# Optimization experiments

Measured on AMD Instinct MI355X. Metric: run time of the kernel, lower is better.

The kernel has to match this reference:

```python
import jax, jax.numpy as jnp
import numpy as np

HIDDEN = 150

def setup_inputs() -> dict:
    key = jax.random.key(0)
    ks = jax.random.split(key, 6)
    B, N, E = 1, 512, 256
    G = 3 * E  # gij_dim = 768
    embeds = jax.random.normal(ks[0], (B, N, E), dtype=jnp.float32)
    mention_scores = jax.random.normal(ks[1], (B, N, 1), dtype=jnp.float32)
    W1 = jax.random.normal(ks[2], (G, HIDDEN), dtype=jnp.float32) * (1.0 / np.sqrt(G))
    b1 = jnp.zeros((HIDDEN,), dtype=jnp.float32)
    W2 = jax.random.normal(ks[3], (HIDDEN, HIDDEN), dtype=jnp.float32) * (1.0 / np.sqrt(HIDDEN))
    b2 = jnp.zeros((HIDDEN,), dtype=jnp.float32)
    W3 = jax.random.normal(ks[4], (HIDDEN, 1), dtype=jnp.float32) * (1.0 / np.sqrt(HIDDEN))
    b3 = jnp.zeros((1,), dtype=jnp.float32)
    return {"batch_document_span_embeds": embeds, "mention_scores": mention_scores,
            "W1": W1, "b1": b1, "W2": W2, "b2": b2, "W3": W3, "b3": b3}


def reference(batch_document_span_embeds, mention_scores, W1, b1, W2, b2, W3, b3):
    g = batch_document_span_embeds            # [B, N, E]
    gi = g[:, :, None, :]                     # span_1 broadcast -> [B, N, 1, E]
    gj = g[:, None, :, :]                     # span_2 broadcast -> [B, 1, N, E]
    B, N, E = g.shape
    # pairwise feature cat((s1, s2, s1*s2)) -> [B, N, N, 3E]
    pair = jnp.concatenate([
        jnp.broadcast_to(gi, (B, N, N, E)),
        jnp.broadcast_to(gj, (B, N, N, E)),
        gi * gj,
    ], axis=-1)
    # small MLP score (dropout is inference-mode identity)
    h = jax.nn.relu(pair @ W1 + b1)           # [B, N, N, 150]
    h = jax.nn.relu(h @ W2 + b2)              # [B, N, N, 150]
    s = h @ W3 + b3                           # [B, N, N, 1]
    # mean of (mention_i, mention_j, pair_ij)
    out = (mention_scores[:, :, None, :] + mention_scores[:, None, :, :] + s) / 3.0
    return out                                # [B, N, N, 1]
```

## Files before the change

kernel.cpp:

```cpp
#include <hip/hip_runtime.h>

#define N  512
#define E  256
#define H  150
#define HP 160
#define JB 64
#define NCH (N / JB)

typedef __attribute__((ext_vector_type(8))) short short8;
typedef __attribute__((ext_vector_type(4))) float f32x4;
typedef __attribute__((ext_vector_type(4))) unsigned uint4v;
typedef __attribute__((ext_vector_type(2))) unsigned uint2v;

__device__ __forceinline__ unsigned short f2bf(float f) {
    unsigned u = __float_as_uint(f);
    u += 0x7fffu + ((u >> 16) & 1u);
    return (unsigned short)(u >> 16);
}
__device__ __forceinline__ unsigned pkbf(float a, float b) {
    return (unsigned)f2bf(a) | ((unsigned)f2bf(b) << 16);
}

__global__ __launch_bounds__(192) void precompute_ab(
    const float* __restrict__ g, const float* __restrict__ W1,
    const float* __restrict__ b1, float* __restrict__ wsA,
    unsigned short* __restrict__ wsB)
{
    const int i0  = blockIdx.x * 4;
    const int tid = threadIdx.x;
    __shared__ float gi[4][E];
    for (int idx = tid; idx < 4 * E; idx += 192) gi[idx >> 8][idx & 255] = g[i0 * E + idx];
    __syncthreads();
    const int h = tid;
    if (h < HP) {
        float a[4] = {0, 0, 0, 0}, b[4] = {0, 0, 0, 0};
        if (h < H) {
            for (int e = 0; e < E; ++e) {
                const float wa = W1[e * H + h];
                const float wb = W1[(E + e) * H + h];
#pragma unroll
                for (int qq = 0; qq < 4; ++qq) {
                    a[qq] = fmaf(gi[qq][e], wa, a[qq]);
                    b[qq] = fmaf(gi[qq][e], wb, b[qq]);
                }
            }
            const float bb = b1[h];
#pragma unroll
            for (int qq = 0; qq < 4; ++qq) a[qq] += bb;
        }
#pragma unroll
        for (int qq = 0; qq < 4; ++qq) {
            wsA[(i0 + qq) * HP + h] = a[qq];
            wsB[(i0 + qq) * HP + h] = f2bf(b[qq]);
        }
    }
}

#define OFF_P   0
#define OFF_H1  33792
#define OFF_C2  55296
#define OFF_W3L 55936
#define OFF_SB  56576
#define LDS_SZ  57600

__global__ __launch_bounds__(512, 2) void pairwise_mfma(
    const float* __restrict__ g,  const float* __restrict__ ms,
    const float* __restrict__ W1, const float* __restrict__ W2,
    const float* __restrict__ b2, const float* __restrict__ W3,
    const float* __restrict__ b3, const float* __restrict__ wsA,
    const unsigned short* __restrict__ wsB, float* __restrict__ out)
{
    __shared__ __attribute__((aligned(16))) char smem[LDS_SZ];
    float* smf = (float*)smem;
    const int tid  = threadIdx.x;
    const int wave = tid >> 6;
    const int lane = tid & 63;
    const int c    = lane & 15;
    const int q    = lane >> 4;
    const int wq   = wave & 3;
    const int jh   = wave >> 2;
    const int hbase  = (wq < 2) ? wq * 48 : 96 + (wq - 2) * 32;
    const int mcount = (wq < 2) ? 3 : 2;
    const short8 z8 = {0, 0, 0, 0, 0, 0, 0, 0};

    short8 w1f[3][8];
    for (int p = 0; p < 2; ++p) {
        if (p) __syncthreads();
        if (tid < 300) {
            const int h = (tid < 150) ? tid : tid - 150;
            const int half = (tid < 150) ? 0 : 1;
            const float* wsrc = W1 + (2 * E + p * 128) * H + h;
            char* dst = smem + h * 272 + half * 128;
#pragma unroll 4
            for (int t = 0; t < 32; ++t) {
                const int ep = half * 32 + t;
                *(unsigned*)(dst + t * 4) = pkbf(wsrc[(2 * ep) * H], wsrc[(2 * ep + 1) * H]);
            }
        }
        __syncthreads();
#pragma unroll
        for (int m = 0; m < 3; ++m) {
            const int hr = hbase + m * 16 + c;
#pragma unroll
            for (int ktp = 0; ktp < 4; ++ktp)
                w1f[m][p * 4 + ktp] = (m < mcount && hr < H)
                    ? *(const short8*)(smem + hr * 272 + (ktp * 32 + q * 8) * 2) : z8;
        }
    }
    __syncthreads();
    if (tid < 300) {
        const int h = (tid < 150) ? tid : tid - 150;
        const int half = (tid < 150) ? 0 : 1;
        char* dst = smem + h * 336;
#pragma unroll 4
        for (int t = 0; t < 42; ++t) {
            const int kp = half * 42 + t;
            const float lo = (2 * kp     < H) ? W2[(2 * kp) * H + h]     : 0.0f;
            const float hi = (2 * kp + 1 < H) ? W2[(2 * kp + 1) * H + h] : 0.0f;
            *(unsigned*)(dst + kp * 4) = pkbf(lo, hi);
        }
    }
    if (tid >= 320 && tid < 480) {
        const int hx = tid - 320;
        smf[OFF_C2 / 4 + hx]  = (hx < H) ? b2[hx] : 0.0f;
        smf[OFF_W3L / 4 + hx] = (hx < H) ? W3[hx] : 0.0f;
    }
    __syncthreads();
    short8 w2f[3][5];
#pragma unroll
    for (int m = 0; m < 3; ++m) {
        const int hr = hbase + m * 16 + c;
#pragma unroll
        for (int kt = 0; kt < 5; ++kt)
            w2f[m][kt] = (m < mcount && hr < H)
                ? *(const short8*)(smem + hr * 336 + (kt * 32 + q * 8) * 2) : z8;
    }
    __syncthreads();

    const int jb = tid >> 5;
    const int e0 = (tid & 31) * 8;
    const float b3v = b3[0];

    const int i = blockIdx.x;
    const f32x4 ga = *(const f32x4*)(g + i * E + e0);
    const f32x4 gb = *(const f32x4*)(g + i * E + e0 + 4);
    f32x4 av[3];
#pragma unroll
    for (int m = 0; m < 3; ++m)
        av[m] = (m < mcount) ? *(const f32x4*)(wsA + i * HP + hbase + m * 16 + q * 4)
                             : (f32x4){0, 0, 0, 0};
    const float msi = ms[i];

    for (int ch = 0; ch < NCH; ++ch) {
        const int j0 = ch * JB;
#pragma unroll
        for (int it = 0; it < 4; ++it) {
            const int jl = jb + it * 16;
            const float* gr = g + (j0 + jl) * E + e0;
            const f32x4 u = *(const f32x4*)gr;
            const f32x4 v = *(const f32x4*)(gr + 4);
            uint4v pk;
            pk[0] = pkbf(u[0] * ga[0], u[1] * ga[1]);
            pk[1] = pkbf(u[2] * ga[2], u[3] * ga[3]);
            pk[2] = pkbf(v[0] * gb[0], v[1] * gb[1]);
            pk[3] = pkbf(v[2] * gb[2], v[3] * gb[3]);
            *(uint4v*)(smem + OFF_P + jl * 528 + e0 * 2) = pk;
        }
        __syncthreads();

        f32x4 acc[2][3];
#pragma unroll
        for (int jt = 0; jt < 2; ++jt)
#pragma unroll
            for (int m = 0; m < 3; ++m) acc[jt][m] = (f32x4){0, 0, 0, 0};
#pragma unroll
        for (int kt = 0; kt < 8; ++kt) {
            short8 pf[2];
#pragma unroll
            for (int jt = 0; jt < 2; ++jt)
                pf[jt] = *(const short8*)(smem + OFF_P + (jh * 32 + jt * 16 + c) * 528 + (kt * 32 + q * 8) * 2);
#pragma unroll
            for (int m = 0; m < 3; ++m)
                if (m < mcount)
#pragma unroll
                    for (int jt = 0; jt < 2; ++jt)
                        acc[jt][m] = __builtin_amdgcn_mfma_f32_16x16x32_bf16(w1f[m][kt], pf[jt], acc[jt][m], 0, 0, 0);
        }
#pragma unroll
        for (int m = 0; m < 3; ++m)
            if (m < mcount) {
                const int h0 = hbase + m * 16 + q * 4;
#pragma unroll
                for (int jt = 0; jt < 2; ++jt) {
                    const int j = jh * 32 + jt * 16 + c;
                    const uint2v bv = *(const uint2v*)(wsB + (j0 + j) * HP + h0);
                    const float v0 = fmaxf(acc[jt][m][0] + av[m][0] + __uint_as_float(bv[0] << 16), 0.0f);
                    const float v1 = fmaxf(acc[jt][m][1] + av[m][1] + __uint_as_float(bv[0] & 0xffff0000u), 0.0f);
                    const float v2 = fmaxf(acc[jt][m][2] + av[m][2] + __uint_as_float(bv[1] << 16), 0.0f);
                    const float v3 = fmaxf(acc[jt][m][3] + av[m][3] + __uint_as_float(bv[1] & 0xffff0000u), 0.0f);
                    uint2v hw;
                    hw[0] = pkbf(v0, v1);
                    hw[1] = pkbf(v2, v3);
                    *(uint2v*)(smem + OFF_H1 + j * 336 + h0 * 2) = hw;
                }
            }
        __syncthreads();

#pragma unroll
        for (int jt = 0; jt < 2; ++jt)
#pragma unroll
            for (int m = 0; m < 3; ++m) acc[jt][m] = (f32x4){0, 0, 0, 0};
#pragma unroll
        for (int kt = 0; kt < 5; ++kt) {
            short8 hf[2];
#pragma unroll
            for (int jt = 0; jt < 2; ++jt)
                hf[jt] = *(const short8*)(smem + OFF_H1 + (jh * 32 + jt * 16 + c) * 336 + (kt * 32 + q * 8) * 2);
#pragma unroll
            for (int m = 0; m < 3; ++m)
                if (m < mcount)
#pragma unroll
                    for (int jt = 0; jt < 2; ++jt)
                        acc[jt][m] = __builtin_amdgcn_mfma_f32_16x16x32_bf16(w2f[m][kt], hf[jt], acc[jt][m], 0, 0, 0);
        }
        float part[2] = {0.0f, 0.0f};
#pragma unroll
        for (int m = 0; m < 3; ++m)
            if (m < mcount) {
                const int h0 = hbase + m * 16 + q * 4;
                const f32x4 b2v = *(const f32x4*)(smf + OFF_C2 / 4 + h0);
                const f32x4 w3v = *(const f32x4*)(smf + OFF_W3L / 4 + h0);
#pragma unroll
                for (int jt = 0; jt < 2; ++jt)
#pragma unroll
                    for (int r = 0; r < 4; ++r)
                        part[jt] = fmaf(fmaxf(acc[jt][m][r] + b2v[r], 0.0f), w3v[r], part[jt]);
            }
#pragma unroll
        for (int jt = 0; jt < 2; ++jt) {
            float pv = part[jt];
            pv += __shfl_xor(pv, 16);
            pv += __shfl_xor(pv, 32);
            if (q == 0) smf[OFF_SB / 4 + wq * 64 + jh * 32 + jt * 16 + c] = pv;
        }
        __syncthreads();
        if (tid < JB) {
            const int j = j0 + tid;
            const float s = smf[OFF_SB / 4 + tid] + smf[OFF_SB / 4 + 64 + tid]
                          + smf[OFF_SB / 4 + 128 + tid] + smf[OFF_SB / 4 + 192 + tid] + b3v;
            out[i * N + j] = (msi + ms[j] + s) * (1.0f / 3.0f);
        }
    }
}

extern "C" void kernel_launch(void* const* d_in, const int* in_sizes, int n_in,
                              void* d_out, int out_size, void* d_ws, size_t ws_size,
                              hipStream_t stream) {
    const float* g  = (const float*)d_in[0];
    const float* ms = (const float*)d_in[1];
    const float* W1 = (const float*)d_in[2];
    const float* b1 = (const float*)d_in[3];
    const float* W2 = (const float*)d_in[4];
    const float* b2 = (const float*)d_in[5];
    const float* W3 = (const float*)d_in[6];
    const float* b3 = (const float*)d_in[7];
    float* out = (float*)d_out;
    float* wsA = (float*)d_ws;
    unsigned short* wsB = (unsigned short*)((char*)d_ws + N * HP * 4);

    precompute_ab<<<N / 4, 192, 0, stream>>>(g, W1, b1, wsA, wsB);
    pairwise_mfma<<<N, 512, 0, stream>>>(g, ms, W1, W2, b2, W3, b3, wsA, wsB, out);
}
```

Baseline: 179.6 us.

## Process two rows i per block, sharing j-row loads and deferring output writes

Each block now handles two query rows i instead of one, with waves split by row (is) rather than by j-half. Each loaded g[j] row is reused to build pair products for both rows, and weight setup is amortised over twice the work. Per-chunk partial scores are kept in LDS and all outputs are written once at the end. LDS grows to about 128 KB via dynamic shared memory, which likely cuts occupancy to one block per CU and halves the grid to 256 blocks.

```diff
diff --git a/kernel.cpp b/kernel.cpp
--- a/kernel.cpp
+++ b/kernel.cpp
@@ -56,12 +56,14 @@
     }
 }
 
-#define OFF_P   0
-#define OFF_H1  33792
-#define OFF_C2  55296
-#define OFF_W3L 55936
-#define OFF_SB  56576
-#define LDS_SZ  57600
+#define OFF_P0   0
+#define OFF_P1   33792
+#define OFF_H10  67584
+#define OFF_H11  89088
+#define OFF_SB   110592
+#define OFF_C2   126976
+#define OFF_W3L  127616
+#define LDS_SZ   128256
 
 __global__ __launch_bounds__(512, 2) void pairwise_mfma(
     const float* __restrict__ g,  const float* __restrict__ ms,
@@ -70,15 +72,16 @@
     const float* __restrict__ b3, const float* __restrict__ wsA,
     const unsigned short* __restrict__ wsB, float* __restrict__ out)
 {
-    __shared__ __attribute__((aligned(16))) char smem[LDS_SZ];
+    extern __shared__ __attribute__((aligned(16))) char smem[];
     float* smf = (float*)smem;
     const int tid  = threadIdx.x;
     const int wave = tid >> 6;
     const int lane = tid & 63;
     const int c    = lane & 15;
     const int q    = lane >> 4;
-    const int wq   = wave & 3;
-    const int jh   = wave >> 2;
+    const int is   = wave >> 2;
+    const int wqr  = wave & 3;
+    const int wq   = is ? (3 - wqr) : wqr;
     const int hbase  = (wq < 2) ? wq * 48 : 96 + (wq - 2) * 32;
     const int mcount = (wq < 2) ? 3 : 2;
     const short8 z8 = {0, 0, 0, 0, 0, 0, 0, 0};
@@ -140,16 +143,22 @@
     const int jb = tid >> 5;
     const int e0 = (tid & 31) * 8;
     const float b3v = b3[0];
-
-    const int i = blockIdx.x;
-    const f32x4 ga = *(const f32x4*)(g + i * E + e0);
-    const f32x4 gb = *(const f32x4*)(g + i * E + e0 + 4);
+    const int i0 = blockIdx.x * 2;
+    const int i  = i0 + is;
+
+    const f32x4 ga0 = *(const f32x4*)(g + i0 * E + e0);
+    const f32x4 gb0 = *(const f32x4*)(g + i0 * E + e0 + 4);
+    const f32x4 ga1 = *(const f32x4*)(g + (i0 + 1) * E + e0);
+    const f32x4 gb1 = *(const f32x4*)(g + (i0 + 1) * E + e0 + 4);
+
     f32x4 av[3];
 #pragma unroll
     for (int m = 0; m < 3; ++m)
         av[m] = (m < mcount) ? *(const f32x4*)(wsA + i * HP + hbase + m * 16 + q * 4)
                              : (f32x4){0, 0, 0, 0};
-    const float msi = ms[i];
+
+    const int offP = is ? OFF_P1  : OFF_P0;
+    const int offH = is ? OFF_H11 : OFF_H10;
 
     for (int ch = 0; ch < NCH; ++ch) {
         const int j0 = ch * JB;
@@ -160,95 +169,114 @@
             const f32x4 u = *(const f32x4*)gr;
             const f32x4 v = *(const f32x4*)(gr + 4);
             uint4v pk;
-            pk[0] = pkbf(u[0] * ga[0], u[1] * ga[1]);
-            pk[1] = pkbf(u[2] * ga[2], u[3] * ga[3]);
-            pk[2] = pkbf(v[0] * gb[0], v[1] * gb[1]);
-            pk[3] = pkbf(v[2] * gb[2], v[3] * gb[3]);
-            *(uint4v*)(smem + OFF_P + jl * 528 + e0 * 2) = pk;
+            pk[0] = pkbf(u[0] * ga0[0], u[1] * ga0[1]);
+            pk[1] = pkbf(u[2] * ga0[2], u[3] * ga0[3]);
+            pk[2] = pkbf(v[0] * gb0[0], v[1] * gb0[1]);
+            pk[3] = pkbf(v[2] * gb0[2], v[3] * gb0[3]);
+            *(uint4v*)(smem + OFF_P0 + jl * 528 + e0 * 2) = pk;
+            pk[0] = pkbf(u[0] * ga1[0], u[1] * ga1[1]);
+            pk[1] = pkbf(u[2] * ga1[2], u[3] * ga1[3]);
+            pk[2] = pkbf(v[0] * gb1[0], v[1] * gb1[1]);
+            pk[3] = pkbf(v[2] * gb1[2], v[3] * gb1[3]);
+            *(uint4v*)(smem + OFF_P1 + jl * 528 + e0 * 2) = pk;
         }
         __syncthreads();
 
-        f32x4 acc[2][3];
-#pragma unroll
-        for (int jt = 0; jt < 2; ++jt)
-#pragma unroll
-            for (int m = 0; m < 3; ++m) acc[jt][m] = (f32x4){0, 0, 0, 0};
-#pragma unroll
-        for (int kt = 0; kt < 8; ++kt) {
-            short8 pf[2];
+#pragma unroll
+        for (int jp = 0; jp < 2; ++jp) {
+            f32x4 acc[2][3];
 #pragma unroll
             for (int jt = 0; jt < 2; ++jt)
-                pf[jt] = *(const short8*)(smem + OFF_P + (jh * 32 + jt * 16 + c) * 528 + (kt * 32 + q * 8) * 2);
+#pragma unroll
+                for (int m = 0; m < 3; ++m) acc[jt][m] = (f32x4){0, 0, 0, 0};
+#pragma unroll
+            for (int kt = 0; kt < 8; ++kt) {
+                short8 pf[2];
+#pragma unroll
+                for (int jt = 0; jt < 2; ++jt)
+                    pf[jt] = *(const short8*)(smem + offP + ((jp * 2 + jt) * 16 + c) * 528 + (kt * 32 + q * 8) * 2);
+#pragma unroll
+                for (int m = 0; m < 3; ++m)
+                    if (m < mcount)
+#pragma unroll
+                        for (int jt = 0; jt < 2; ++jt)
+                            acc[jt][m] = __builtin_amdgcn_mfma_f32_16x16x32_bf16(w1f[m][kt], pf[jt], acc[jt][m], 0, 0, 0);
+            }
 #pragma unroll
             for (int m = 0; m < 3; ++m)
-                if (m < mcount)
+                if (m < mcount) {
+                    const int h0 = hbase + m * 16 + q * 4;
+#pragma unroll
+                    for (int jt = 0; jt < 2; ++jt) {
+                        const int j = (jp * 2 + jt) * 16 + c;
+                        const uint2v bv = *(const uint2v*)(wsB + (j0 + j) * HP + h0);
+                        const float v0 = fmaxf(acc[jt][m][0] + av[m][0] + __uint_as_float(bv[0] << 16), 0.0f);
+                        const float v1 = fmaxf(acc[jt][m][1] + av[m][1] + __uint_as_float(bv[0] & 0xffff0000u), 0.0f);
+                        const float v2 = fmaxf(acc[jt][m][2] + av[m][2] + __uint_as_float(bv[1] << 16), 0.0f);
+                        const float v3 = fmaxf(acc[jt][m][3] + av[m][3] + __uint_as_float(bv[1] & 0xffff0000u), 0.0f);
+                        uint2v hw;
+                        hw[0] = pkbf(v0, v1);
+                        hw[1] = pkbf(v2, v3);
+                        *(uint2v*)(smem + offH + j * 336 + h0 * 2) = hw;
+                    }
+                }
+        }
+        __syncthreads();
+
+#pragma unroll
+        for (int jp = 0; jp < 2; ++jp) {
+            f32x4 acc[2][3];
+#pragma unroll
+            for (int jt = 0; jt < 2; ++jt)
+#pragma unroll
+                for (int m = 0; m < 3; ++m) acc[jt][m] = (f32x4){0, 0, 0, 0};
+#pragma unroll
+            for (int kt = 0; kt < 5; ++kt) {
+                short8 hf[2];
+#pragma unroll
+                for (int jt = 0; jt < 2; ++jt)
+                    hf[jt] = *(const short8*)(smem + offH + ((jp * 2 + jt) * 16 + c) * 336 + (kt * 32 + q * 8) * 2);
+#pragma unroll
+                for (int m = 0; m < 3; ++m)
+                    if (m < mcount)
+#pragma unroll
+                        for (int jt = 0; jt < 2; ++jt)
+                            acc[jt][m] = __builtin_amdgcn_mfma_f32_16x16x32_bf16(w2f[m][kt], hf[jt], acc[jt][m], 0, 0, 0);
+            }
+            float part[2] = {0.0f, 0.0f};
+#pragma unroll
+            for (int m = 0; m < 3; ++m)
+                if (m < mcount) {
+                    const int h0 = hbase + m * 16 + q * 4;
+                    const f32x4 b2v = *(const f32x4*)(smf + OFF_C2 / 4 + h0);
+                    const f32x4 w3v = *(const f32x4*)(smf + OFF_W3L / 4 + h0);
 #pragma unroll
                     for (int jt = 0; jt < 2; ++jt)
-                        acc[jt][m] = __builtin_amdgcn_mfma_f32_16x16x32_bf16(w1f[m][kt], pf[jt], acc[jt][m], 0, 0, 0);
-        }
-#pragma unroll
-        for (int m = 0; m < 3; ++m)
-            if (m < mcount) {
-                const int h0 = hbase + m * 16 + q * 4;
-#pragma unroll
-                for (int jt = 0; jt < 2; ++jt) {
-                    const int j = jh * 32 + jt * 16 + c;
-                    const uint2v bv = *(const uint2v*)(wsB + (j0 + j) * HP + h0);
-                    const float v0 = fmaxf(acc[jt][m][0] + av[m][0] + __uint_as_float(bv[0] << 16), 0.0f);
-                    const float v1 = fmaxf(acc[jt][m][1] + av[m][1] + __uint_as_float(bv[0] & 0xffff0000u), 0.0f);
-                    const float v2 = fmaxf(acc[jt][m][2] + av[m][2] + __uint_as_float(bv[1] << 16), 0.0f);
-                    const float v3 = fmaxf(acc[jt][m][3] + av[m][3] + __uint_as_float(bv[1] & 0xffff0000u), 0.0f);
-                    uint2v hw;
-                    hw[0] = pkbf(v0, v1);
-                    hw[1] = pkbf(v2, v3);
-                    *(uint2v*)(smem + OFF_H1 + j * 336 + h0 * 2) = hw;
+#pragma unroll
+                        for (int r = 0; r < 4; ++r)
+                            part[jt] = fmaf(fmaxf(acc[jt][m][r] + b2v[r], 0.0f), w3v[r], part[jt]);
                 }
-            }
+#pragma unroll
+            for (int jt = 0; jt < 2; ++jt) {
+                float pv = part[jt];
+                pv += __shfl_xor(pv, 16);
+                pv += __shfl_xor(pv, 32);
+                if (q == 0)
+                    smf[OFF_SB / 4 + ((is * 8 + ch) * 4 + wq) * 64 + (jp * 2 + jt) * 16 + c] = pv;
+            }
+        }
         __syncthreads();
-
-#pragma unroll
-        for (int jt = 0; jt < 2; ++jt)
-#pragma unroll
-            for (int m = 0; m < 3; ++m) acc[jt][m] = (f32x4){0, 0, 0, 0};
-#pragma unroll
-        for (int kt = 0; kt < 5; ++kt) {
-            short8 hf[2];
-#pragma unroll
-            for (int jt = 0; jt < 2; ++jt)
-                hf[jt] = *(const short8*)(smem + OFF_H1 + (jh * 32 + jt * 16 + c) * 336 + (kt * 32 + q * 8) * 2);
-#pragma unroll
-            for (int m = 0; m < 3; ++m)
-                if (m < mcount)
-#pragma unroll
-                    for (int jt = 0; jt < 2; ++jt)
-                        acc[jt][m] = __builtin_amdgcn_mfma_f32_16x16x32_bf16(w2f[m][kt], hf[jt], acc[jt][m], 0, 0, 0);
-        }
-        float part[2] = {0.0f, 0.0f};
-#pragma unroll
-        for (int m = 0; m < 3; ++m)
-            if (m < mcount) {
-                const int h0 = hbase + m * 16 + q * 4;
-                const f32x4 b2v = *(const f32x4*)(smf + OFF_C2 / 4 + h0);
-                const f32x4 w3v = *(const f32x4*)(smf + OFF_W3L / 4 + h0);
-#pragma unroll
-                for (int jt = 0; jt < 2; ++jt)
-#pragma unroll
-                    for (int r = 0; r < 4; ++r)
-                        part[jt] = fmaf(fmaxf(acc[jt][m][r] + b2v[r], 0.0f), w3v[r], part[jt]);
-            }
-#pragma unroll
-        for (int jt = 0; jt < 2; ++jt) {
-            float pv = part[jt];
-            pv += __shfl_xor(pv, 16);
-            pv += __shfl_xor(pv, 32);
-            if (q == 0) smf[OFF_SB / 4 + wq * 64 + jh * 32 + jt * 16 + c] = pv;
-        }
-        __syncthreads();
-        if (tid < JB) {
-            const int j = j0 + tid;
-            const float s = smf[OFF_SB / 4 + tid] + smf[OFF_SB / 4 + 64 + tid]
-                          + smf[OFF_SB / 4 + 128 + tid] + smf[OFF_SB / 4 + 192 + tid] + b3v;
-            out[i * N + j] = (msi + ms[j] + s) * (1.0f / 3.0f);
+    }
+
+    {
+        const float msj = ms[tid];
+        const int chf = tid >> 6, jl = tid & 63;
+#pragma unroll
+        for (int is2 = 0; is2 < 2; ++is2) {
+            const int iw = i0 + is2;
+            const int base = OFF_SB / 4 + ((is2 * 8 + chf) * 4) * 64 + jl;
+            const float s = smf[base] + smf[base + 64] + smf[base + 128] + smf[base + 192] + b3v;
+            out[iw * N + tid] = (ms[iw] + msj + s) * (1.0f / 3.0f);
         }
     }
 }
@@ -268,6 +296,13 @@
     float* wsA = (float*)d_ws;
     unsigned short* wsB = (unsigned short*)((char*)d_ws + N * HP * 4);
 
+    static bool attr_set = false;
+    if (!attr_set) {
+        hipFuncSetAttribute((const void*)pairwise_mfma,
+                            hipFuncAttributeMaxDynamicSharedMemorySize, LDS_SZ);
+        attr_set = true;
+    }
+
     precompute_ab<<<N / 4, 192, 0, stream>>>(g, W1, b1, wsA, wsB);
-    pairwise_mfma<<<N, 512, 0, stream>>>(g, ms, W1, W2, b2, W3, b3, wsA, wsB, out);
-}
+    pairwise_mfma<<<N / 2, 512, LDS_SZ, stream>>>(g, ms, W1, W2, b2, W3, b3, wsA, wsB, out);
+}
```

Measured after the change: 164.1 us. -8.6%, faster.
